# Kernel tuning notes

Measured on AMD Instinct MI355X. Metric: run time of the kernel, lower is better.

The kernel has to match this reference:

```python
import jax, jax.numpy as jnp
import numpy as np

B, C, K, H, W = 64, 512, 64, 64, 64
EPS = 1e-12  # torch F.normalize eps


def setup_inputs() -> dict:
    key = jax.random.key(0)
    k1, k2, k3, k4 = jax.random.split(key, 4)
    x = jax.random.normal(k1, (B, C, H, W), dtype=jnp.float32)
    conv_w = jax.random.normal(k2, (K, C), dtype=jnp.float32) * 0.1  # 1x1 conv weight, squeezed
    conv_b = jax.random.normal(k3, (K,), dtype=jnp.float32) * 0.1
    centroids = jax.random.normal(k4, (K, C), dtype=jnp.float32)
    return {"x": x, "conv_w": conv_w, "conv_b": conv_b, "centroids": centroids}


def _l2norm(v, axis):
    n = jnp.sqrt(jnp.sum(v * v, axis=axis, keepdims=True))
    return v / jnp.maximum(n, EPS)


def reference(x, conv_w, conv_b, centroids):
    b, c, h, w = x.shape
    k = centroids.shape[0]
    hw = h * w
    # F.normalize(x, p=2, dim=1)
    xn = _l2norm(x, axis=1)
    # 1x1 conv -> [b,k,h,w] -> [b,k,hw], softmax over clusters
    logits = jnp.einsum('bchw,kc->bkhw', xn, conv_w) + conv_b[None, :, None, None]
    soft_assign = jax.nn.softmax(logits.reshape(b, k, hw), axis=1)
    # faithful to original: x.view(b, -1, c) with NO permute (channel-major reinterpretation)
    x_flatten = xn.reshape(b, hw, c)
    # vlad[b,k,c] = sum_i a[b,k,i] * (xf[b,i,c] - cent[k,c])
    vlad = (jnp.einsum('bki,bic->bkc', soft_assign, x_flatten)
            - jnp.sum(soft_assign, axis=2)[:, :, None] * centroids[None])
    vlad = _l2norm(vlad, axis=2)            # intra-normalize per cluster
    vlad = vlad.reshape(b, -1)
    vlad = _l2norm(vlad, axis=1)            # global L2 normalize
    return vlad
```

## Files before the change

kernel.cpp:

```cpp
#include <hip/hip_runtime.h>

#define HW 4096
#define NC 512
#define NK 64
#define NB 64

typedef unsigned short u16;
typedef float  float4v __attribute__((ext_vector_type(4)));
typedef short  short8  __attribute__((ext_vector_type(8)));

__device__ __forceinline__ u16 f2bf(float f){
  unsigned u = __builtin_bit_cast(unsigned, f);
  u += 0x7fffu + ((u >> 16) & 1u);
  return (u16)(u >> 16);
}
__device__ __forceinline__ unsigned pk2(float a, float b){
  return (unsigned)f2bf(a) | ((unsigned)f2bf(b) << 16);
}

__global__ __launch_bounds__(256) void nv_k1(
    const float* __restrict__ x, const float* __restrict__ w,
    const float* __restrict__ bias, float* __restrict__ invnorm,
    u16* __restrict__ a_out, float* __restrict__ asum)
{
  __shared__ u16 w_sh[NK * 40];
  __shared__ u16 x_sh[256 * 40];
  __shared__ float bias_sh[NK];

  const int t    = threadIdx.x;
  const int b    = blockIdx.y;
  const int p0   = blockIdx.x * 256;
  const int wave = t >> 6, lane = t & 63, q = lane >> 4, l16 = lane & 15;

  if (t < NK) bias_sh[t] = bias[t];

  const float* xb = x + (size_t)b * NC * HW;
  float sumsq = 0.f;

  float4v acc[4][4];
  const float4v zf = {0.f, 0.f, 0.f, 0.f};
  #pragma unroll
  for (int i = 0; i < 4; ++i)
    #pragma unroll
    for (int j = 0; j < 4; ++j) acc[i][j] = zf;

  for (int step = 0; step < 16; ++step){
    const int c0 = step * 32;
    __syncthreads();
    {
      const int m = t >> 2, cq = (t & 3) * 8;
      const float* wp = w + m * NC + c0 + cq;
      float4 w0 = *(const float4*)wp;
      float4 w1 = *(const float4*)(wp + 4);
      uint4 pk;
      pk.x = pk2(w0.x, w0.y); pk.y = pk2(w0.z, w0.w);
      pk.z = pk2(w1.x, w1.y); pk.w = pk2(w1.z, w1.w);
      *(uint4*)&w_sh[m * 40 + cq] = pk;
    }
    {
      const float* xp = xb + (size_t)c0 * HW + p0 + t;
      #pragma unroll
      for (int c8 = 0; c8 < 4; ++c8){
        float v0 = xp[(c8*8+0)*HW], v1 = xp[(c8*8+1)*HW];
        float v2 = xp[(c8*8+2)*HW], v3 = xp[(c8*8+3)*HW];
        float v4 = xp[(c8*8+4)*HW], v5 = xp[(c8*8+5)*HW];
        float v6 = xp[(c8*8+6)*HW], v7 = xp[(c8*8+7)*HW];
        sumsq += v0*v0 + v1*v1 + v2*v2 + v3*v3 + v4*v4 + v5*v5 + v6*v6 + v7*v7;
        uint4 pk;
        pk.x = pk2(v0, v1); pk.y = pk2(v2, v3);
        pk.z = pk2(v4, v5); pk.w = pk2(v6, v7);
        *(uint4*)&x_sh[t * 40 + c8 * 8] = pk;
      }
    }
    __syncthreads();
    short8 av[4], bv[4];
    #pragma unroll
    for (int ms = 0; ms < 4; ++ms)
      av[ms] = *(const short8*)&w_sh[(ms*16 + l16) * 40 + q*8];
    #pragma unroll
    for (int ns = 0; ns < 4; ++ns)
      bv[ns] = *(const short8*)&x_sh[(wave*64 + ns*16 + l16) * 40 + q*8];
    #pragma unroll
    for (int ms = 0; ms < 4; ++ms)
      #pragma unroll
      for (int ns = 0; ns < 4; ++ns)
        acc[ms][ns] = __builtin_amdgcn_mfma_f32_16x16x32_bf16(av[ms], bv[ns], acc[ms][ns], 0, 0, 0);
  }

  float inv = 1.f / fmaxf(sqrtf(sumsq), 1e-12f);
  invnorm[(size_t)b * HW + p0 + t] = inv;

  float inv_n[4];
  #pragma unroll
  for (int ns = 0; ns < 4; ++ns) inv_n[ns] = __shfl(inv, ns*16 + l16, 64);

  #pragma unroll
  for (int ns = 0; ns < 4; ++ns){
    float mx = -3.4e38f;
    #pragma unroll
    for (int ms = 0; ms < 4; ++ms)
      #pragma unroll
      for (int r = 0; r < 4; ++r){
        float lv = fmaf(acc[ms][ns][r], inv_n[ns], bias_sh[ms*16 + q*4 + r]);
        acc[ms][ns][r] = lv;
        mx = fmaxf(mx, lv);
      }
    mx = fmaxf(mx, __shfl_xor(mx, 16, 64));
    mx = fmaxf(mx, __shfl_xor(mx, 32, 64));
    float s = 0.f;
    #pragma unroll
    for (int ms = 0; ms < 4; ++ms)
      #pragma unroll
      for (int r = 0; r < 4; ++r){
        float e = __expf(acc[ms][ns][r] - mx);
        acc[ms][ns][r] = e;
        s += e;
      }
    s += __shfl_xor(s, 16, 64);
    s += __shfl_xor(s, 32, 64);
    float is = 1.f / s;
    #pragma unroll
    for (int ms = 0; ms < 4; ++ms)
      #pragma unroll
      for (int r = 0; r < 4; ++r) acc[ms][ns][r] *= is;
  }

  u16* ap = a_out + (size_t)b * NK * HW + p0 + wave * 64;
  #pragma unroll
  for (int ms = 0; ms < 4; ++ms)
    #pragma unroll
    for (int r = 0; r < 4; ++r){
      const int m = ms*16 + q*4 + r;
      #pragma unroll
      for (int ns = 0; ns < 4; ++ns)
        ap[(size_t)m * HW + ns*16 + l16] = f2bf(acc[ms][ns][r]);
    }

  #pragma unroll
  for (int ms = 0; ms < 4; ++ms)
    #pragma unroll
    for (int r = 0; r < 4; ++r){
      const int m = ms*16 + q*4 + r;
      float s = acc[ms][0][r] + acc[ms][1][r] + acc[ms][2][r] + acc[ms][3][r];
      s += __shfl_xor(s, 1, 64); s += __shfl_xor(s, 2, 64);
      s += __shfl_xor(s, 4, 64); s += __shfl_xor(s, 8, 64);
      if (l16 == 0) atomicAdd(&asum[b * NK + m], s);
    }
}

__global__ __launch_bounds__(256) void nv_k2(
    const float* __restrict__ x, const u16* __restrict__ a_buf,
    const float* __restrict__ invnorm, float* __restrict__ vpart)
{
  __shared__ u16 a_sh[NK * 40];

  const int t    = threadIdx.x;
  const int b    = blockIdx.z;
  const int iq   = blockIdx.y;
  const int cc0  = blockIdx.x * 256;
  const int wave = t >> 6, lane = t & 63, q = lane >> 4, l16 = lane & 15;

  const int cbase = cc0 + wave * 64 + l16;

  const float* invb = invnorm + (size_t)b * HW;
  float invr[4][8];
  #pragma unroll
  for (int ns = 0; ns < 4; ++ns)
    #pragma unroll
    for (int j = 0; j < 8; ++j)
      invr[ns][j] = invb[j * 512 + cbase + ns * 16];

  const float* xb  = x + (size_t)b * NC * HW;
  const u16*   ab  = a_buf + (size_t)b * NK * HW + iq * 1024;
  const float* xpb = xb + (size_t)(iq * 128 + q) * HW + cbase;

  float4v acc[4][4];
  const float4v zf = {0.f, 0.f, 0.f, 0.f};
  #pragma unroll
  for (int i = 0; i < 4; ++i)
    #pragma unroll
    for (int j = 0; j < 4; ++j) acc[i][j] = zf;

  for (int step = 0; step < 32; ++step){
    const int i0 = step * 32;
    __syncthreads();
    {
      const int k = t >> 2, i8 = (t & 3) * 8;
      *(float4*)&a_sh[k * 40 + i8] = *(const float4*)&ab[(size_t)k * HW + i0 + i8];
    }
    __syncthreads();
    short8 av[4];
    #pragma unroll
    for (int ms = 0; ms < 4; ++ms)
      av[ms] = *(const short8*)&a_sh[(ms*16 + l16) * 40 + q*8];

    const float* xs = xpb + (size_t)step * 4 * HW;
    #pragma unroll
    for (int ns = 0; ns < 4; ++ns){
      float v[8];
      #pragma unroll
      for (int j = 0; j < 8; ++j)
        v[j] = xs[j * 512 + ns * 16] * invr[ns][j];
      short8 bv;
      #pragma unroll
      for (int j = 0; j < 4; ++j)
        ((unsigned*)&bv)[j] = pk2(v[2*j], v[2*j+1]);
      #pragma unroll
      for (int ms = 0; ms < 4; ++ms)
        acc[ms][ns] = __builtin_amdgcn_mfma_f32_16x16x32_bf16(av[ms], bv, acc[ms][ns], 0, 0, 0);
    }
  }

  float* vp = vpart + (size_t)(iq * NB + b) * NK * NC;
  #pragma unroll
  for (int ms = 0; ms < 4; ++ms)
    #pragma unroll
    for (int ns = 0; ns < 4; ++ns)
      #pragma unroll
      for (int r = 0; r < 4; ++r){
        const int m = ms*16 + q*4 + r;
        const int n = cc0 + wave*64 + ns*16 + l16;
        vp[(size_t)m * NC + n] = acc[ms][ns][r];
      }
}

__global__ __launch_bounds__(256) void nv_k3a(
    const float* __restrict__ vpart, const float* __restrict__ asum,
    const float* __restrict__ cent, float* __restrict__ vlad,
    float* __restrict__ rstat)
{
  __shared__ float part_sh[256];
  const int b = blockIdx.x, t = threadIdx.x;
  const int k = t >> 2, seg = t & 3;
  const size_t roff = ((size_t)b * NK + k) * NC + seg * 128;
  const size_t bstride = (size_t)NB * NK * NC;
  const float* p0 = vpart + roff;
  const float as = asum[b * NK + k];
  const float* cp = cent + k * NC + seg * 128;
  float* vp = vlad + roff;

  float s = 0.f;
  #pragma unroll 4
  for (int j = 0; j < 32; ++j){
    float4 a0 = *(const float4*)&p0[j*4];
    float4 a1 = *(const float4*)&p0[bstride + j*4];
    float4 a2 = *(const float4*)&p0[2*bstride + j*4];
    float4 a3 = *(const float4*)&p0[3*bstride + j*4];
    float4 c4 = *(const float4*)&cp[j*4];
    float4 v;
    v.x = (a0.x + a1.x) + (a2.x + a3.x) - as * c4.x;
    v.y = (a0.y + a1.y) + (a2.y + a3.y) - as * c4.y;
    v.z = (a0.z + a1.z) + (a2.z + a3.z) - as * c4.z;
    v.w = (a0.w + a1.w) + (a2.w + a3.w) - as * c4.w;
    *(float4*)&vp[j*4] = v;
    s += v.x*v.x + v.y*v.y + v.z*v.z + v.w*v.w;
  }
  part_sh[t] = s;
  __syncthreads();
  if (t < NK){
    float rs = part_sh[t*4] + part_sh[t*4+1] + part_sh[t*4+2] + part_sh[t*4+3];
    float ri = 1.f / fmaxf(sqrtf(rs), 1e-12f);
    rstat[b * 128 + t]      = ri;
    rstat[b * 128 + 64 + t] = rs * ri * ri;
  }
}

__global__ __launch_bounds__(256) void nv_k3c(
    const float* __restrict__ vlad, const float* __restrict__ rstat,
    float* __restrict__ out)
{
  __shared__ float rinv_sh[NK];
  __shared__ float gsh;
  const int b = blockIdx.x, t = threadIdx.x;
  if (t < 64){
    float ri = rstat[b * 128 + t];
    rinv_sh[t] = ri;
    float sk = rstat[b * 128 + 64 + t];
    sk += __shfl_xor(sk, 1, 64);  sk += __shfl_xor(sk, 2, 64);
    sk += __shfl_xor(sk, 4, 64);  sk += __shfl_xor(sk, 8, 64);
    sk += __shfl_xor(sk, 16, 64); sk += __shfl_xor(sk, 32, 64);
    if (t == 0) gsh = 1.f / fmaxf(sqrtf(sk), 1e-12f);
  }
  __syncthreads();
  const float g = gsh;
  const float* vb = vlad + (size_t)b * NK * NC;
  float* ob = out + (size_t)b * NK * NC;
  #pragma unroll 4
  for (int j = 0; j < 32; ++j){
    const int idx = j * 1024 + t * 4;
    float4 v = *(const float4*)&vb[idx];
    float sc = rinv_sh[idx >> 9] * g;
    float4 o; o.x = v.x*sc; o.y = v.y*sc; o.z = v.z*sc; o.w = v.w*sc;
    *(float4*)&ob[idx] = o;
  }
}

extern "C" void kernel_launch(void* const* d_in, const int* in_sizes, int n_in,
                              void* d_out, int out_size, void* d_ws, size_t ws_size,
                              hipStream_t stream)
{
  (void)in_sizes; (void)n_in; (void)out_size; (void)ws_size;
  const float* x    = (const float*)d_in[0];
  const float* w    = (const float*)d_in[1];
  const float* bias = (const float*)d_in[2];
  const float* cent = (const float*)d_in[3];
  float* out = (float*)d_out;

  char* ws = (char*)d_ws;
  float* invnorm = (float*)ws;
  u16*   a_buf   = (u16*)(ws + (1u  << 20));
  float* asum    = (float*)(ws + (33u << 20));
  float* rstat   = (float*)(ws + (33u << 20) + 65536u);
  float* vlad    = (float*)(ws + (34u << 20));
  float* vpart   = (float*)(ws + (42u << 20));

  hipMemsetAsync(asum, 0, NB * NK * sizeof(float), stream);
  hipLaunchKernelGGL(nv_k1, dim3(16, 64), dim3(256), 0, stream,
                     x, w, bias, invnorm, a_buf, asum);
  hipLaunchKernelGGL(nv_k2, dim3(2, 4, 64), dim3(256), 0, stream,
                     x, a_buf, invnorm, vpart);
  hipLaunchKernelGGL(nv_k3a, dim3(64), dim3(256), 0, stream,
                     vpart, asum, cent, vlad, rstat);
  hipLaunchKernelGGL(nv_k3c, dim3(64), dim3(256), 0, stream,
                     vlad, rstat, out);
}
```

Measured before the change: 835.9 us.

## Widen the finalize kernels' grids and move the k2 inverse norms into shared memory

The two final normalization kernels now launch 4 blocks per batch instead of 1. Each kernel handles 16 clusters per block with coalesced float4 strides, and the k3a row-norm reduction now uses wave shuffles instead of shared memory. This spreads the memory-bound vpart/vlad passes over far more compute units. In the main accumulation kernel, the per-thread 32-register cache of inverse norms moves to shared memory and a minimum-occupancy launch bound is added, trading extra LDS reads for lower register pressure.

```diff
diff --git a/kernel.cpp b/kernel.cpp
--- a/kernel.cpp
+++ b/kernel.cpp
@@ -148,11 +148,12 @@
     }
 }
 
-__global__ __launch_bounds__(256) void nv_k2(
+__global__ __launch_bounds__(256, 3) void nv_k2(
     const float* __restrict__ x, const u16* __restrict__ a_buf,
     const float* __restrict__ invnorm, float* __restrict__ vpart)
 {
   __shared__ u16 a_sh[NK * 40];
+  __shared__ float inv_sh[8 * 256];
 
   const int t    = threadIdx.x;
   const int b    = blockIdx.z;
@@ -160,19 +161,16 @@
   const int cc0  = blockIdx.x * 256;
   const int wave = t >> 6, lane = t & 63, q = lane >> 4, l16 = lane & 15;
 
-  const int cbase = cc0 + wave * 64 + l16;
+  const int cl = wave * 64 + l16;
 
   const float* invb = invnorm + (size_t)b * HW;
-  float invr[4][8];
-  #pragma unroll
-  for (int ns = 0; ns < 4; ++ns)
-    #pragma unroll
-    for (int j = 0; j < 8; ++j)
-      invr[ns][j] = invb[j * 512 + cbase + ns * 16];
+  #pragma unroll
+  for (int j = 0; j < 8; ++j)
+    inv_sh[j * 256 + t] = invb[j * 512 + cc0 + t];
 
   const float* xb  = x + (size_t)b * NC * HW;
   const u16*   ab  = a_buf + (size_t)b * NK * HW + iq * 1024;
-  const float* xpb = xb + (size_t)(iq * 128 + q) * HW + cbase;
+  const float* xpb = xb + (size_t)(iq * 128 + q) * HW + cc0 + wave * 64 + l16;
 
   float4v acc[4][4];
   const float4v zf = {0.f, 0.f, 0.f, 0.f};
@@ -200,7 +198,7 @@
       float v[8];
       #pragma unroll
       for (int j = 0; j < 8; ++j)
-        v[j] = xs[j * 512 + ns * 16] * invr[ns][j];
+        v[j] = xs[j * 512 + ns * 16] * inv_sh[j * 256 + cl + ns * 16];
       short8 bv;
       #pragma unroll
       for (int j = 0; j < 4; ++j)
@@ -229,39 +227,38 @@
     const float* __restrict__ cent, float* __restrict__ vlad,
     float* __restrict__ rstat)
 {
-  __shared__ float part_sh[256];
-  const int b = blockIdx.x, t = threadIdx.x;
-  const int k = t >> 2, seg = t & 3;
-  const size_t roff = ((size_t)b * NK + k) * NC + seg * 128;
+  const int b = blockIdx.y, kg = blockIdx.x, t = threadIdx.x;
+  const int k = kg * 16 + (t >> 4), seg = t & 15;
+  const size_t roff = ((size_t)b * NK + k) * NC + seg * 4;
   const size_t bstride = (size_t)NB * NK * NC;
   const float* p0 = vpart + roff;
   const float as = asum[b * NK + k];
-  const float* cp = cent + k * NC + seg * 128;
+  const float* cp = cent + (size_t)k * NC + seg * 4;
   float* vp = vlad + roff;
 
   float s = 0.f;
-  #pragma unroll 4
-  for (int j = 0; j < 32; ++j){
-    float4 a0 = *(const float4*)&p0[j*4];
-    float4 a1 = *(const float4*)&p0[bstride + j*4];
-    float4 a2 = *(const float4*)&p0[2*bstride + j*4];
-    float4 a3 = *(const float4*)&p0[3*bstride + j*4];
-    float4 c4 = *(const float4*)&cp[j*4];
+  #pragma unroll
+  for (int j = 0; j < 8; ++j){
+    const int o = j * 64;
+    float4 a0 = *(const float4*)&p0[o];
+    float4 a1 = *(const float4*)&p0[bstride + o];
+    float4 a2 = *(const float4*)&p0[2*bstride + o];
+    float4 a3 = *(const float4*)&p0[3*bstride + o];
+    float4 c4 = *(const float4*)&cp[o];
     float4 v;
     v.x = (a0.x + a1.x) + (a2.x + a3.x) - as * c4.x;
     v.y = (a0.y + a1.y) + (a2.y + a3.y) - as * c4.y;
     v.z = (a0.z + a1.z) + (a2.z + a3.z) - as * c4.z;
     v.w = (a0.w + a1.w) + (a2.w + a3.w) - as * c4.w;
-    *(float4*)&vp[j*4] = v;
+    *(float4*)&vp[o] = v;
     s += v.x*v.x + v.y*v.y + v.z*v.z + v.w*v.w;
   }
-  part_sh[t] = s;
-  __syncthreads();
-  if (t < NK){
-    float rs = part_sh[t*4] + part_sh[t*4+1] + part_sh[t*4+2] + part_sh[t*4+3];
-    float ri = 1.f / fmaxf(sqrtf(rs), 1e-12f);
-    rstat[b * 128 + t]      = ri;
-    rstat[b * 128 + 64 + t] = rs * ri * ri;
+  s += __shfl_xor(s, 1, 64); s += __shfl_xor(s, 2, 64);
+  s += __shfl_xor(s, 4, 64); s += __shfl_xor(s, 8, 64);
+  if (seg == 0){
+    float ri = 1.f / fmaxf(sqrtf(s), 1e-12f);
+    rstat[b * 128 + k]      = ri;
+    rstat[b * 128 + 64 + k] = s * ri * ri;
   }
 }
 
@@ -269,24 +266,24 @@
     const float* __restrict__ vlad, const float* __restrict__ rstat,
     float* __restrict__ out)
 {
-  __shared__ float rinv_sh[NK];
+  __shared__ float rinv_sh[16];
   __shared__ float gsh;
-  const int b = blockIdx.x, t = threadIdx.x;
+  const int b = blockIdx.y, qg = blockIdx.x, t = threadIdx.x;
   if (t < 64){
-    float ri = rstat[b * 128 + t];
-    rinv_sh[t] = ri;
     float sk = rstat[b * 128 + 64 + t];
     sk += __shfl_xor(sk, 1, 64);  sk += __shfl_xor(sk, 2, 64);
     sk += __shfl_xor(sk, 4, 64);  sk += __shfl_xor(sk, 8, 64);
     sk += __shfl_xor(sk, 16, 64); sk += __shfl_xor(sk, 32, 64);
     if (t == 0) gsh = 1.f / fmaxf(sqrtf(sk), 1e-12f);
+  } else if (t < 80){
+    rinv_sh[t - 64] = rstat[b * 128 + qg * 16 + (t - 64)];
   }
   __syncthreads();
   const float g = gsh;
-  const float* vb = vlad + (size_t)b * NK * NC;
-  float* ob = out + (size_t)b * NK * NC;
-  #pragma unroll 4
-  for (int j = 0; j < 32; ++j){
+  const float* vb = vlad + (size_t)b * NK * NC + qg * 8192;
+  float* ob = out + (size_t)b * NK * NC + qg * 8192;
+  #pragma unroll
+  for (int j = 0; j < 8; ++j){
     const int idx = j * 1024 + t * 4;
     float4 v = *(const float4*)&vb[idx];
     float sc = rinv_sh[idx >> 9] * g;
@@ -319,8 +316,8 @@
                      x, w, bias, invnorm, a_buf, asum);
   hipLaunchKernelGGL(nv_k2, dim3(2, 4, 64), dim3(256), 0, stream,
                      x, a_buf, invnorm, vpart);
-  hipLaunchKernelGGL(nv_k3a, dim3(64), dim3(256), 0, stream,
+  hipLaunchKernelGGL(nv_k3a, dim3(4, 64), dim3(256), 0, stream,
                      vpart, asum, cent, vlad, rstat);
-  hipLaunchKernelGGL(nv_k3c, dim3(64), dim3(256), 0, stream,
+  hipLaunchKernelGGL(nv_k3c, dim3(4, 64), dim3(256), 0, stream,
                      vlad, rstat, out);
 }
```

Measured after the change: 804.7 us. 3.7% less time.
